# Performance work log

Hardware: AMD Instinct MI355X
Metric: run time of the kernel (lower is better)

## Reference

```python
import jax, jax.numpy as jnp
import numpy as np
import math

B, N, D, H = 4, 2048, 1024, 16
d = D // H
F = 2048                      # field_size
PAD = 8192                    # _next_fast_size(4*F) = 2^13
FB = PAD // 2 + 1             # rfft freq bins
NC = 32                       # spectral-gate control points
EPS = 1e-6                    # feature-map positivity floor


def setup_inputs():
    key = jax.random.key(0)
    ks = jax.random.split(key, 16)
    rn = lambda k, sh, s=0.02: (jax.random.normal(k, sh) * s).astype(jnp.float32)
    eye = jnp.eye(d, dtype=jnp.float32)
    n = jnp.arange(H, dtype=jnp.float32)
    return {
        "x": jax.random.normal(ks[0], (B, N, D), dtype=jnp.float32),
        "w_qkvg": rn(ks[1], (4 * D, D)),
        "b_qkvg": jnp.concatenate([jnp.zeros(3 * D), jnp.full((D,), 2.0)]).astype(jnp.float32),
        "w_out": rn(ks[2], (D, D)),
        "b_out": jnp.zeros((D,), jnp.float32),
        "qfm_w": jnp.stack([eye + rn(ks[3], (d, d)), eye + rn(ks[4], (d, d))]),
        "qfm_b": jnp.zeros((2, d), jnp.float32),
        "kfm_w": jnp.stack([eye + rn(ks[5], (d, d)), eye + rn(ks[6], (d, d))]),
        "kfm_b": jnp.zeros((2, d), jnp.float32),
        "wg_w": rn(ks[7], (1, d)),
        "wg_b": jnp.zeros((1,), jnp.float32),
        "ln_g": jnp.ones((d,), jnp.float32),
        "ln_b": jnp.zeros((d,), jnp.float32),
        "sg_w1": rn(ks[8], (D, D)),
        "sg_b1": jnp.zeros((D,), jnp.float32),
        "sg_w2": rn(ks[9], (H * NC, D), 0.001),
        "sg_b2": jnp.zeros((H * NC,), jnp.float32),
        "wave_freq": (math.pi * (2 * n + 1) / 2).astype(jnp.float32),
        "wave_damp": jnp.full((H,), -0.69, jnp.float32),
        "wave_phase": jnp.linspace(0.0, math.pi, H).astype(jnp.float32),
        "coupling": (jnp.eye(H, dtype=jnp.float32) + rn(ks[10], (H, H), 0.01)),
    }


def _featmap(x, w, b):
    # Hedgehog-style learned positive feature map: depth x (Linear -> ReLU), + eps
    for i in range(w.shape[0]):
        x = jax.nn.relu(x @ w[i].T + b[i])
    return x + EPS


def reference(x, w_qkvg, b_qkvg, w_out, b_out, qfm_w, qfm_b, kfm_w, kfm_b,
              wg_w, wg_b, ln_g, ln_b, sg_w1, sg_b1, sg_w2, sg_b2,
              wave_freq, wave_damp, wave_phase, coupling):
    # fused qkvg projection -> per-head tensors (B,H,N,d)
    qkvg = x @ w_qkvg.T + b_qkvg
    q, k, v, g = [t.reshape(B, N, H, d).transpose(0, 2, 1, 3)
                  for t in jnp.split(qkvg, 4, axis=-1)]
    phi_q = _featmap(q, qfm_w, qfm_b)
    phi_k = _featmap(k, kfm_w, kfm_b)
    wg = jax.nn.sigmoid(k @ wg_w.T + wg_b)  # (B,H,N,1) write gate

    # token -> field position mapping (cached buffers in the original)
    stride = (F - 1) / max(N - 1, 1)
    pos = jnp.clip(jnp.arange(N, dtype=jnp.float32) * stride, 0, F - 2)
    lo = jnp.clip(pos.astype(jnp.int32), 0, F - 2)
    hi = lo + 1
    frac = jnp.clip(pos - lo.astype(jnp.float32), 0.0, 1.0)

    # scatter numerator (gated phi_k*v) + denominator (gated phi_k) streams
    write = jnp.concatenate([wg * phi_k * v, wg * phi_k], axis=-1)  # (B,H,N,2d)
    field = jnp.zeros((B, H, F, 2 * d), jnp.float32)
    field = field.at[:, :, lo, :].add(write * (1.0 - frac)[:, None])
    field = field.at[:, :, hi, :].add(write * frac[:, None])

    # left-aligned causal damped-wave kernel per head
    t = jnp.arange(F, dtype=jnp.float32) / F
    kern = jnp.exp(-jnp.exp(wave_damp)[:, None] * t) * \
           jnp.cos(wave_freq[:, None] * t + wave_phase[:, None])  # (H,F)
    base_fft = jnp.fft.rfft(kern, n=PAD, axis=-1)                 # (H,FB) complex

    # content-adaptive spectral gate from token 0 (causally safe)
    q0 = q[:, :, 0, :]
    mu = q0.mean(-1, keepdims=True)
    var = q0.var(-1, keepdims=True)
    q0 = (q0 - mu) / jnp.sqrt(var + 1e-5) * ln_g + ln_b
    h1 = jax.nn.gelu(q0.reshape(B, H * d) @ sg_w1.T + sg_b1)
    ctrl = (h1 @ sg_w2.T + sg_b2).reshape(B, H, NC)
    ip = jnp.arange(FB, dtype=jnp.float32) * (NC - 1) / (FB - 1)  # align_corners=True
    il = jnp.clip(ip.astype(jnp.int32), 0, NC - 2)
    iw = ip - il.astype(jnp.float32)
    gate = ctrl[:, :, il] * (1.0 - iw) + ctrl[:, :, il + 1] * iw  # (B,H,FB)
    mod = base_fft[None] * (1.0 + gate)                           # (B,H,FB) complex

    # FFT-domain global convolution + head coupling
    conv = jnp.fft.irfft(jnp.fft.rfft(field, n=PAD, axis=2) * mod[..., None],
                         n=PAD, axis=2)[:, :, :F, :]
    conv = jnp.einsum('hg,bgfc->bhfc', coupling, conv)

    # linear-interp read-back at token positions
    y = conv[:, :, lo, :] * (1.0 - frac)[:, None] + conv[:, :, hi, :] * frac[:, None]
    y_num, y_den = y[..., :d], y[..., d:]
    den = jnp.abs(jnp.sum(phi_q * y_den, axis=-1, keepdims=True)) + 1e-4
    out_h = (phi_q * y_num / den) * jax.nn.sigmoid(g)
    return out_h.transpose(0, 2, 1, 3).reshape(B, N, D) @ w_out.T + b_out
```

## Files before the change

### kernel.cpp

```cpp
#include <hip/hip_runtime.h>
#include <math.h>

#define B_   4
#define N_   2048
#define D_   1024
#define H_   16
#define d_   64
#define F_   2048
#define PAD_ 8192
#define FB_  4097
#define NC_  32
#define EPS_ 1e-6f
#define PI_F 3.14159265358979323846f
#define PI_D 3.14159265358979323846

typedef unsigned short ushort_t;
typedef short bf16x8 __attribute__((ext_vector_type(8)));
typedef float f32x4  __attribute__((ext_vector_type(4)));

#define GLD16(gp, lp) __builtin_amdgcn_global_load_lds( \
    (const __attribute__((address_space(1))) unsigned int*)(const void*)(gp), \
    (__attribute__((address_space(3))) unsigned int*)(void*)(lp), 16, 0, 0)

__device__ __forceinline__ ushort_t bf16_rne(float v) {
    unsigned b = __float_as_uint(v);
    unsigned rb = b + 0x7fffu + ((b >> 16) & 1u);
    return (ushort_t)(rb >> 16);
}
__device__ __forceinline__ void split_bf16(float v, ushort_t& h, ushort_t& l) {
    h = bf16_rne(v);
    float fh = __uint_as_float((unsigned)h << 16);
    l = bf16_rne(v - fh);
}

__device__ __forceinline__ float2 cmul(float2 a, float2 w) {
    return make_float2(a.x * w.x - a.y * w.y, a.x * w.y + a.y * w.x);
}
__device__ __forceinline__ float2 cmulc(float2 a, float2 w) {
    return make_float2(a.x * w.x + a.y * w.y, a.y * w.x - a.x * w.y);
}

__global__ __launch_bounds__(256) void kern_twid(float2* __restrict__ twid,
                                                 float2* __restrict__ tw4) {
    int idx = blockIdx.x * 256 + threadIdx.x;
    if (idx < 13 * 4096) {
        const int lh = idx >> 12, t = idx & 4095;
        const int hh = 1 << lh;
        const int j = t & (hh - 1);
        double s, c;
        sincos(-PI_D * (double)j / (double)hh, &s, &c);
        twid[idx] = make_float2((float)c, (float)s);
    } else {
        idx -= 13 * 4096;
        if (idx < 6 * 3072) {
            const int s = idx / 3072;
            const int r = idx - s * 3072;
            const int j = r / 3;
            const int m = r - 3 * j + 1;
            const int q = 1024 >> (2 * s);
            double sn, cs;
            sincos(-2.0 * PI_D * (double)(m * (j & (q - 1))) / (double)(4 * q), &sn, &cs);
            tw4[idx] = make_float2((float)cs, (float)sn);
        }
    }
}

__global__ __launch_bounds__(256) void kern_split3(
        const float* __restrict__ s0, ushort_t* __restrict__ h0, ushort_t* __restrict__ l0, int n0,
        const float* __restrict__ s1, ushort_t* __restrict__ h1, ushort_t* __restrict__ l1, int n1,
        const float* __restrict__ s2, ushort_t* __restrict__ h2, ushort_t* __restrict__ l2, int n2) {
    int i = blockIdx.x * 256 + threadIdx.x;
    const float* s; ushort_t* hh; ushort_t* ll; int k;
    if (i < n0)                { s = s0; hh = h0; ll = l0; k = i; }
    else if (i < n0 + n1)      { s = s1; hh = h1; ll = l1; k = i - n0; }
    else if (i < n0 + n1 + n2) { s = s2; hh = h2; ll = l2; k = i - n0 - n1; }
    else return;
    ushort_t h, l;
    split_bf16(s[k], h, l);
    hh[k] = h; ll[k] = l;
}

__global__ __launch_bounds__(256) void gemm_mfma(
        const ushort_t* __restrict__ Ah, const ushort_t* __restrict__ Al, int lda,
        const ushort_t* __restrict__ Bh, const ushort_t* __restrict__ Bl, int ldb,
        const float* __restrict__ bias, float* __restrict__ C,
        int Nn, int K) {
    __shared__ __align__(16) ushort_t At0[128 * 32];
    __shared__ __align__(16) ushort_t At1[128 * 32];
    __shared__ __align__(16) ushort_t Bt0[128 * 32];
    __shared__ __align__(16) ushort_t Bt1[128 * 32];

    const int tid = threadIdx.x;
    const int wv = tid >> 6, lane = tid & 63;
    const int quad = lane >> 4, lrow = lane & 15;
    const int m0 = blockIdx.y * 128, n0 = blockIdx.x * 128;
    const int mw = (wv >> 1) * 64, nw = (wv & 1) * 64;

    const int srow = lane >> 2;
    const int schunk = (((lane & 3) ^ ((lane >> 3) & 3)) * 8);
    const int qsw = ((quad ^ ((lrow >> 1) & 3)) * 8);

    f32x4 acc[4][4] = {};

    for (int k0 = 0; k0 < K; k0 += 32) {
        {
            const size_t ga = (size_t)(m0 + wv * 32 + srow) * lda + k0 + schunk;
            const size_t gb = (size_t)(n0 + wv * 32 + srow) * ldb + k0 + schunk;
            const size_t ga2 = ga + (size_t)16 * lda;
            const size_t gb2 = gb + (size_t)16 * ldb;
            GLD16(Ah + ga,  &At0[(wv * 32) * 32]);
            GLD16(Ah + ga2, &At0[(wv * 32 + 16) * 32]);
            GLD16(Al + ga,  &At1[(wv * 32) * 32]);
            GLD16(Al + ga2, &At1[(wv * 32 + 16) * 32]);
            GLD16(Bh + gb,  &Bt0[(wv * 32) * 32]);
            GLD16(Bh + gb2, &Bt0[(wv * 32 + 16) * 32]);
            GLD16(Bl + gb,  &Bt1[(wv * 32) * 32]);
            GLD16(Bl + gb2, &Bt1[(wv * 32 + 16) * 32]);
        }
        __syncthreads();

        bf16x8 a0[4], a1[4], b0[4], b1[4];
#pragma unroll
        for (int i = 0; i < 4; ++i) {
            a0[i] = *(const bf16x8*)&At0[(mw + i * 16 + lrow) * 32 + qsw];
            a1[i] = *(const bf16x8*)&At1[(mw + i * 16 + lrow) * 32 + qsw];
            b0[i] = *(const bf16x8*)&Bt0[(nw + i * 16 + lrow) * 32 + qsw];
            b1[i] = *(const bf16x8*)&Bt1[(nw + i * 16 + lrow) * 32 + qsw];
        }
#pragma unroll
        for (int mi = 0; mi < 4; ++mi)
#pragma unroll
            for (int nj = 0; nj < 4; ++nj) {
                acc[mi][nj] = __builtin_amdgcn_mfma_f32_16x16x32_bf16(a0[mi], b0[nj], acc[mi][nj], 0, 0, 0);
                acc[mi][nj] = __builtin_amdgcn_mfma_f32_16x16x32_bf16(a0[mi], b1[nj], acc[mi][nj], 0, 0, 0);
                acc[mi][nj] = __builtin_amdgcn_mfma_f32_16x16x32_bf16(a1[mi], b0[nj], acc[mi][nj], 0, 0, 0);
            }
        __syncthreads();
    }

#pragma unroll
    for (int mi = 0; mi < 4; ++mi) {
        const int row = m0 + mw + mi * 16 + quad * 4;
#pragma unroll
        for (int nj = 0; nj < 4; ++nj) {
            const int col = n0 + nw + nj * 16 + lrow;
            const float bv = bias[col];
#pragma unroll
            for (int r = 0; r < 4; ++r)
                C[(size_t)(row + r) * Nn + col] = acc[mi][nj][r] + bv;
        }
    }
}

__device__ __forceinline__ float gelu_f(float x) {
    return 0.5f * x * (1.f + tanhf(0.7978845608028654f * (x + 0.044715f * x * x * x)));
}

__global__ __launch_bounds__(256) void kern_gemv4(const float* __restrict__ A,
                                                  const float* __restrict__ W,
                                                  const float* __restrict__ bias,
                                                  float* __restrict__ C,
                                                  int Nn, int act) {
    const int tid = threadIdx.x;
    const int wv = tid >> 6, lane = tid & 63;
    const int col = blockIdx.x * 4 + wv;
    const float* wp = W + (size_t)col * D_;
    float a0 = 0.f, a1 = 0.f, a2 = 0.f, a3 = 0.f;
#pragma unroll
    for (int i = 0; i < 16; ++i) {
        int k = lane + i * 64;
        float w = wp[k];
        a0 += A[k] * w;
        a1 += A[D_ + k] * w;
        a2 += A[2 * D_ + k] * w;
        a3 += A[3 * D_ + k] * w;
    }
    for (int m = 1; m < 64; m <<= 1) {
        a0 += __shfl_xor(a0, m);
        a1 += __shfl_xor(a1, m);
        a2 += __shfl_xor(a2, m);
        a3 += __shfl_xor(a3, m);
    }
    if (lane == 0) {
        float bv = bias[col];
        float v0 = a0 + bv, v1 = a1 + bv, v2 = a2 + bv, v3 = a3 + bv;
        if (act) { v0 = gelu_f(v0); v1 = gelu_f(v1); v2 = gelu_f(v2); v3 = gelu_f(v3); }
        C[0 * Nn + col] = v0;
        C[1 * Nn + col] = v1;
        C[2 * Nn + col] = v2;
        C[3 * Nn + col] = v3;
    }
}

__global__ __launch_bounds__(256) void kern_feat(float* __restrict__ qkvg,
                                                 const float* __restrict__ qfm_w,
                                                 const float* __restrict__ qfm_b,
                                                 const float* __restrict__ kfm_w,
                                                 const float* __restrict__ kfm_b,
                                                 const float* __restrict__ wg_w,
                                                 const float* __restrict__ wg_b,
                                                 float* __restrict__ field) {
    __shared__ __align__(16) float in_t[64][68];
    __shared__ __align__(16) float tmp[64][68];
    __shared__ __align__(16) float wbuf[64][68];
    __shared__ __align__(16) float bsm[64];
    __shared__ float wsm[64];
    __shared__ float wgbuf[64];

    const int tid = threadIdx.x;
    const int lane = tid & 63, grp = tid >> 6;
    const int n0 = blockIdx.x * 64;
    const int h = blockIdx.y, b = blockIdx.z;
    const size_t rowbase = (size_t)(b * N_ + n0) * 4096;

    const int lr4 = tid >> 4;
    const int lc4 = (tid & 15) * 4;

    const int rg = lane >> 4;
    const int cg4 = (lane & 15) * 4;
    const int rbase = grp * 16 + rg * 4;

#define LOAD64x64(dst, off) \
    for (int it = 0; it < 4; ++it) { \
        int r = lr4 + it * 16; \
        float4 v = *(const float4*)&qkvg[rowbase + (size_t)r * 4096 + (off) + lc4]; \
        *(float4*)&dst[r][lc4] = v; \
    }

#define MLP2_ACC(srcarr) \
    f32x4 acc[4] = {}; \
    for (int c4 = 0; c4 < 64; c4 += 4) { \
        f32x4 wv0 = *(const f32x4*)&wbuf[c4 + 0][cg4]; \
        f32x4 wv1 = *(const f32x4*)&wbuf[c4 + 1][cg4]; \
        f32x4 wv2 = *(const f32x4*)&wbuf[c4 + 2][cg4]; \
        f32x4 wv3 = *(const f32x4*)&wbuf[c4 + 3][cg4]; \
        _Pragma("unroll") for (int rr = 0; rr < 4; ++rr) { \
            f32x4 iv = *(const f32x4*)&srcarr[rbase + rr][c4]; \
            acc[rr] += wv0 * iv[0]; \
            acc[rr] += wv1 * iv[1]; \
            acc[rr] += wv2 * iv[2]; \
            acc[rr] += wv3 * iv[3]; \
        } \
    }

#define MLP2_STORE_LDS(dstarr, EPSV) { \
    f32x4 b4 = *(const f32x4*)&bsm[cg4]; \
    _Pragma("unroll") for (int rr = 0; rr < 4; ++rr) { \
        f32x4 v = acc[rr] + b4; \
        _Pragma("unroll") for (int k = 0; k < 4; ++k) v[k] = fmaxf(v[k], 0.f) + (EPSV); \
        *(f32x4*)&dstarr[rbase + rr][cg4] = v; } }

    LOAD64x64(in_t, D_ + h * 64)
    for (int it = 0; it < 16; ++it) {
        int r = grp + 4 * it;
        wbuf[lane][r] = kfm_w[(size_t)r * 64 + lane];
    }
    if (tid < 64) { bsm[tid] = kfm_b[tid]; wsm[tid] = wg_w[tid]; }
    __syncthreads();
    if (tid < 64) {
        float s = 0.f;
        for (int c4 = 0; c4 < 64; c4 += 4) {
            float4 iv = *(const float4*)&in_t[tid][c4];
            s += iv.x * wsm[c4] + iv.y * wsm[c4 + 1] + iv.z * wsm[c4 + 2] + iv.w * wsm[c4 + 3];
        }
        s += wg_b[0];
        wgbuf[tid] = 1.f / (1.f + expf(-s));
    }
    {
        MLP2_ACC(in_t)
        MLP2_STORE_LDS(tmp, 0.f)
    }
    __syncthreads();
    for (int it = 0; it < 16; ++it) {
        int r = grp + 4 * it;
        wbuf[lane][r] = kfm_w[(size_t)(64 + r) * 64 + lane];
    }
    if (tid < 64) bsm[tid] = kfm_b[64 + tid];
    __syncthreads();
    {
        MLP2_ACC(tmp)
        MLP2_STORE_LDS(in_t, EPS_)
    }
    __syncthreads();
    LOAD64x64(tmp, 2 * D_ + h * 64)
    __syncthreads();

    {
        float* frow = field + (size_t)(b * H_ + h) * 128 * F_;
        const bool last = (n0 == N_ - 64);
        for (int c = grp; c < 128; c += 4) {
            int i = lane;
            float v = (c < 64) ? wgbuf[i] * in_t[i][c] * tmp[i][c]
                               : wgbuf[i] * in_t[i][c - 64];
            if (last) {
                if (i == 62) {
                    float v2 = (c < 64) ? wgbuf[63] * in_t[63][c] * tmp[63][c]
                                        : wgbuf[63] * in_t[63][c - 64];
                    v += v2;
                } else if (i == 63) v = 0.f;
            }
            frow[(size_t)c * F_ + n0 + i] = v;
        }
    }
    __syncthreads();

    LOAD64x64(in_t, h * 64)
    for (int it = 0; it < 16; ++it) {
        int r = grp + 4 * it;
        wbuf[lane][r] = qfm_w[(size_t)r * 64 + lane];
    }
    if (tid < 64) bsm[tid] = qfm_b[tid];
    __syncthreads();
    {
        MLP2_ACC(in_t)
        MLP2_STORE_LDS(tmp, 0.f)
    }
    __syncthreads();
    for (int it = 0; it < 16; ++it) {
        int r = grp + 4 * it;
        wbuf[lane][r] = qfm_w[(size_t)(64 + r) * 64 + lane];
    }
    if (tid < 64) bsm[tid] = qfm_b[64 + tid];
    __syncthreads();
    {
        MLP2_ACC(tmp)
        f32x4 b4 = *(const f32x4*)&bsm[cg4];
#pragma unroll
        for (int rr = 0; rr < 4; ++rr) {
            f32x4 v = acc[rr] + b4;
#pragma unroll
            for (int k = 0; k < 4; ++k) v[k] = fmaxf(v[k], 0.f) + EPS_;
            *(f32x4*)&qkvg[rowbase + (size_t)(rbase + rr) * 4096 + D_ + h * 64 + cg4] = v;
        }
    }
#undef LOAD64x64
#undef MLP2_ACC
#undef MLP2_STORE_LDS
}

__global__ void kern_ln(const float* __restrict__ qkvg,
                        const float* __restrict__ ln_g,
                        const float* __restrict__ ln_b,
                        float* __restrict__ q0n) {
    const int bh = blockIdx.x, c = threadIdx.x;
    const int b = bh >> 4, h = bh & 15;
    float x = qkvg[(size_t)(b * N_) * 4096 + h * 64 + c];
    float mu = x;
    for (int m = 1; m < 64; m <<= 1) mu += __shfl_xor(mu, m);
    mu *= (1.f / 64.f);
    float dv = (x - mu) * (x - mu);
    for (int m = 1; m < 64; m <<= 1) dv += __shfl_xor(dv, m);
    float var = dv * (1.f / 64.f);
    q0n[b * 1024 + h * 64 + c] = (x - mu) * rsqrtf(var + 1e-5f) * ln_g[c] + ln_b[c];
}

template <int NT>
__device__ __forceinline__ void fft_fwd_dif_t(float* xr, float* xi, int tid, int logn,
                                              const float2* __restrict__ twid) {
    const int nb = 1 << (logn - 1);
    for (int lh = logn - 1; lh >= 0; --lh) {
        const int hh = 1 << lh;
        const float2* tws = twid + lh * 4096;
        for (int t = tid; t < nb; t += NT) {
            int j = t & (hh - 1);
            int i1 = ((t >> lh) << (lh + 1)) | j;
            int i2 = i1 + hh;
            float2 tw = tws[t];
            float ar = xr[i1], ai = xi[i1];
            float br = xr[i2], bi = xi[i2];
            xr[i1] = ar + br; xi[i1] = ai + bi;
            float tr = ar - br, ti = ai - bi;
            xr[i2] = tr * tw.x - ti * tw.y;
            xi[i2] = tr * tw.y + ti * tw.x;
        }
        __syncthreads();
    }
}

template <int NT>
__device__ __forceinline__ void fft_inv_dit_t(float* xr, float* xi, int tid, int logn,
                                              const float2* __restrict__ twid) {
    const int nb = 1 << (logn - 1);
    for (int lh = 0; lh < logn; ++lh) {
        const int hh = 1 << lh;
        const float2* tws = twid + lh * 4096;
        for (int t = tid; t < nb; t += NT) {
            int j = t & (hh - 1);
            int i1 = ((t >> lh) << (lh + 1)) | j;
            int i2 = i1 + hh;
            float2 tw = tws[t];
            float br = xr[i2], bi = xi[i2];
            float tr = br * tw.x + bi * tw.y;
            float ti = bi * tw.x - br * tw.y;
            float ar = xr[i1], ai = xi[i1];
            xr[i1] = ar + tr; xi[i1] = ai + ti;
            xr[i2] = ar - tr; xi[i2] = ai - ti;
        }
        __syncthreads();
    }
}

#define ZIDX(i) ((i) + ((i) >> 4))

template <int NT>
__device__ __forceinline__ void fft4_fwd(float2* z, int tid,
                                         const float2* __restrict__ tw4) {
#pragma unroll
    for (int s = 0; s < 6; ++s) {
        const int q = 1024 >> (2 * s);
        const int qq = q + (q >> 4);
        const float2* tws = tw4 + s * 3072;
        for (int t = tid; t < 1024; t += NT) {
            int j = t & (q - 1);
            int base = ((t & ~(q - 1)) << 2) | j;
            int i0, i1, i2, i3;
            if (q >= 16) { i0 = ZIDX(base); i1 = i0 + qq; i2 = i1 + qq; i3 = i2 + qq; }
            else { i0 = ZIDX(base); i1 = ZIDX(base + q); i2 = ZIDX(base + 2 * q); i3 = ZIDX(base + 3 * q); }
            float2 a = z[i0], b = z[i1], c = z[i2], d = z[i3];
            float2 s0 = make_float2(a.x + c.x, a.y + c.y);
            float2 s1 = make_float2(a.x - c.x, a.y - c.y);
            float2 s2 = make_float2(b.x + d.x, b.y + d.y);
            float2 s3 = make_float2(b.x - d.x, b.y - d.y);
            float2 m1 = make_float2(s1.x + s3.y, s1.y - s3.x);
            float2 m2 = make_float2(s0.x - s2.x, s0.y - s2.y);
            float2 m3 = make_float2(s1.x - s3.y, s1.y + s3.x);
            z[i0] = make_float2(s0.x + s2.x, s0.y + s2.y);
            z[i1] = cmul(m1, tws[3 * j + 0]);
            z[i2] = cmul(m2, tws[3 * j + 1]);
            z[i3] = cmul(m3, tws[3 * j + 2]);
        }
        __syncthreads();
    }
}

template <int NT>
__device__ __forceinline__ void fft4_inv(float2* z, int tid,
                                         const float2* __restrict__ tw4) {
#pragma unroll
    for (int s = 5; s >= 0; --s) {
        const int q = 1024 >> (2 * s);
        const int qq = q + (q >> 4);
        const float2* tws = tw4 + s * 3072;
        for (int t = tid; t < 1024; t += NT) {
            int j = t & (q - 1);
            int base = ((t & ~(q - 1)) << 2) | j;
            int i0, i1, i2, i3;
            if (q >= 16) { i0 = ZIDX(base); i1 = i0 + qq; i2 = i1 + qq; i3 = i2 + qq; }
            else { i0 = ZIDX(base); i1 = ZIDX(base + q); i2 = ZIDX(base + 2 * q); i3 = ZIDX(base + 3 * q); }
            float2 a = z[i0];
            float2 b = cmulc(z[i1], tws[3 * j + 0]);
            float2 c = cmulc(z[i2], tws[3 * j + 1]);
            float2 d = cmulc(z[i3], tws[3 * j + 2]);
            float2 p0 = make_float2(a.x + c.x, a.y + c.y);
            float2 p1 = make_float2(a.x - c.x, a.y - c.y);
            float2 p2 = make_float2(b.x + d.x, b.y + d.y);
            float2 p3 = make_float2(b.x - d.x, b.y - d.y);
            z[i0] = make_float2(p0.x + p2.x, p0.y + p2.y);
            z[i1] = make_float2(p1.x - p3.y, p1.y + p3.x);
            z[i2] = make_float2(p0.x - p2.x, p0.y - p2.y);
            z[i3] = make_float2(p1.x + p3.y, p1.y - p3.x);
        }
        __syncthreads();
    }
}

__global__ __launch_bounds__(1024) void kern_prep(const float* __restrict__ freq,
                                                  const float* __restrict__ damp,
                                                  const float* __restrict__ phase,
                                                  const float* __restrict__ ctrl,
                                                  const float2* __restrict__ twid,
                                                  const float2* __restrict__ tw4,
                                                  float* __restrict__ GBR) {
    __shared__ float sm[2 * PAD_];
    float* xr = sm;
    float* xi = sm + PAD_;
    const int bh = blockIdx.x, tid = threadIdx.x;
    const int b = bh >> 4, h = bh & 15;

    const float fr = freq[h], ed = expf(damp[h]), ph = phase[h];
    for (int f = tid; f < PAD_; f += 1024) {
        float v = 0.f;
        if (f < F_) {
            float t = (float)f / (float)F_;
            v = expf(-ed * t) * cosf(fr * t + ph);
        }
        xr[f] = v; xi[f] = 0.f;
    }
    __syncthreads();
    fft_fwd_dif_t<1024>(xr, xi, tid, 13, twid);

    const float* cp = ctrl + b * (H_ * NC_) + h * NC_;
    for (int j = tid; j < PAD_; j += 1024) {
        int k = (int)(__brev((unsigned)j) >> 19);
        int kk = min(k, PAD_ - k);
        float ip = (float)kk * ((float)(NC_ - 1) / (float)(FB_ - 1));
        int il = min((int)ip, NC_ - 2);
        float iw = ip - (float)il;
        float m = 1.f + cp[il] * (1.f - iw) + cp[il + 1] * iw;
        xr[j] *= m;
        xi[j] *= m;
    }
    __syncthreads();
    fft_inv_dit_t<1024>(xr, xi, tid, 13, twid);

    float g[4];
    const float sc = 1.f / (float)PAD_;
#pragma unroll
    for (int u = 0; u < 4; ++u) {
        int j = tid + u * 1024;
        g[u] = ((j < 2048) ? xr[j] : xr[j + 4096]) * sc;
    }
    __syncthreads();
    float2* z = (float2*)sm;
#pragma unroll
    for (int u = 0; u < 4; ++u) {
        int j = tid + u * 1024;
        z[ZIDX(j)] = make_float2(g[u], 0.f);
    }
    __syncthreads();
    fft4_fwd<1024>(z, tid, tw4);
    for (int j = tid; j < 4096; j += 1024) {
        float2 v = z[ZIDX(j)];
        GBR[((size_t)bh * 4096 + j) * 2 + 0] = v.x;
        GBR[((size_t)bh * 4096 + j) * 2 + 1] = v.y;
    }
}

__global__ __launch_bounds__(512) void kern_conv4(float* __restrict__ field,
                                                  const float* __restrict__ GBR,
                                                  const float2* __restrict__ tw4) {
    __shared__ float2 z[4351];
    const int tid = threadIdx.x;
    const int bh = blockIdx.x >> 6, cp = blockIdx.x & 63;
    float* rowx = field + ((size_t)bh * 128 + 2 * cp) * F_;
    float* rowy = rowx + F_;

    for (int f = tid; f < 2048; f += 512) {
        z[ZIDX(f)] = make_float2(rowx[f], rowy[f]);
        z[ZIDX(f + 2048)] = make_float2(0.f, 0.f);
    }
    __syncthreads();

    fft4_fwd<512>(z, tid, tw4);

    {
        const float2* G = (const float2*)(GBR) + (size_t)bh * 4096;
        for (int j = tid; j < 4096; j += 512) {
            int zi = ZIDX(j);
            z[zi] = cmul(z[zi], G[j]);
        }
    }
    __syncthreads();

    fft4_inv<512>(z, tid, tw4);

    const float s = 1.f / 4096.f;
    for (int f = tid; f < 2048; f += 512) {
        float2 v = z[ZIDX(f)];
        rowx[f] = v.x * s;
        rowy[f] = v.y * s;
    }
}

__global__ __launch_bounds__(1024) void kern_combine(float* __restrict__ qkvg,
                                                     const float* __restrict__ field,
                                                     const float* __restrict__ coupling) {
    __shared__ float cpl[16][16];
    __shared__ float sbuf[2][128][17];
    const int tid = threadIdx.x;
    if (tid < 256) cpl[tid >> 4][tid & 15] = coupling[tid];
    const int lane = tid & 63, wv = tid >> 6;
    const int n = blockIdx.x * 16 + wv;
    const int b = blockIdx.y;
    const int f0 = blockIdx.x * 16;
    const int fi = min(n, F_ - 2) - f0;
    const size_t row = (size_t)(b * N_ + n) * 4096;

    const int lc = tid >> 3, lk = (tid & 7) * 2;
    const float* fb = field + (size_t)b * 16 * 128 * F_;

    float2 rv = *(const float2*)&fb[(size_t)lc * F_ + f0 + lk];
    __syncthreads();
    sbuf[0][lc][lk] = rv.x; sbuf[0][lc][lk + 1] = rv.y;

    float ynum[16], yden[16];
#pragma unroll
    for (int hh = 0; hh < 16; ++hh) { ynum[hh] = 0.f; yden[hh] = 0.f; }

    for (int g = 0; g < 16; ++g) {
        if (g < 15)
            rv = *(const float2*)&fb[((size_t)(g + 1) * 128 + lc) * F_ + f0 + lk];
        __syncthreads();
        const float nv = sbuf[g & 1][lane][fi];
        const float dv = sbuf[g & 1][64 + lane][fi];
#pragma unroll
        for (int hh = 0; hh < 16; ++hh) {
            const float cg = cpl[hh][g];
            ynum[hh] += cg * nv;
            yden[hh] += cg * dv;
        }
        if (g < 15) { sbuf[(g + 1) & 1][lc][lk] = rv.x; sbuf[(g + 1) & 1][lc][lk + 1] = rv.y; }
    }

    ushort_t* rp = (ushort_t*)(qkvg + row);
#pragma unroll
    for (int hh = 0; hh < 16; ++hh) {
        float pq = qkvg[row + D_ + hh * 64 + lane];
        float gv = qkvg[row + 3 * D_ + hh * 64 + lane];
        float s = pq * yden[hh];
        for (int m = 1; m < 64; m <<= 1) s += __shfl_xor(s, m);
        float den = fabsf(s) + 1e-4f;
        float o = pq * ynum[hh] / den * (1.f / (1.f + expf(-gv)));
        ushort_t oh, ol;
        split_bf16(o, oh, ol);
        rp[hh * 64 + lane] = oh;
        rp[1024 + hh * 64 + lane] = ol;
    }
}

extern "C" void kernel_launch(void* const* d_in, const int* in_sizes, int n_in,
                              void* d_out, int out_size, void* d_ws, size_t ws_size,
                              hipStream_t stream) {
    const float* x      = (const float*)d_in[0];
    const float* w_qkvg = (const float*)d_in[1];
    const float* b_qkvg = (const float*)d_in[2];
    const float* w_out  = (const float*)d_in[3];
    const float* b_out  = (const float*)d_in[4];
    const float* qfm_w  = (const float*)d_in[5];
    const float* qfm_b  = (const float*)d_in[6];
    const float* kfm_w  = (const float*)d_in[7];
    const float* kfm_b  = (const float*)d_in[8];
    const float* wg_w   = (const float*)d_in[9];
    const float* wg_b   = (const float*)d_in[10];
    const float* ln_g   = (const float*)d_in[11];
    const float* ln_b   = (const float*)d_in[12];
    const float* sg_w1  = (const float*)d_in[13];
    const float* sg_b1  = (const float*)d_in[14];
    const float* sg_w2  = (const float*)d_in[15];
    const float* sg_b2  = (const float*)d_in[16];
    const float* wfreq  = (const float*)d_in[17];
    const float* wdamp  = (const float*)d_in[18];
    const float* wphase = (const float*)d_in[19];
    const float* coup   = (const float*)d_in[20];

    float* ws = (float*)d_ws;
    float*  qkvg   = ws;
    float*  field  = ws + 33554432;
    float*  GBR    = ws + 50593792;
    float2* twid   = (float2*)(ws + 51118080);
    float*  q0n    = ws + 51224576;
    float*  h1     = ws + 51228672;
    float*  ctrl   = ws + 51232768;
    ushort_t* wouth = (ushort_t*)(ws + 51234816);
    ushort_t* woutl = (ushort_t*)(ws + 51759104);
    float2* tw4    = (float2*)(ws + 52283392);

    ushort_t* xh  = (ushort_t*)(field);
    ushort_t* xl  = (ushort_t*)(field + 4194304);
    ushort_t* wqh = (ushort_t*)(field + 8388608);
    ushort_t* wql = (ushort_t*)(field + 10485760);

    kern_twid<<<(13 * 4096 + 6 * 3072) / 256, 256, 0, stream>>>(twid, tw4);
    kern_split3<<<(B_ * N_ * D_ + 4 * D_ * D_ + D_ * D_) / 256, 256, 0, stream>>>(
        x, xh, xl, B_ * N_ * D_,
        w_qkvg, wqh, wql, 4 * D_ * D_,
        w_out, wouth, woutl, D_ * D_);

    gemm_mfma<<<dim3(4096 / 128, 8192 / 128), 256, 0, stream>>>(
        xh, xl, D_, wqh, wql, D_, b_qkvg, qkvg, 4 * D_, D_);

    kern_ln<<<B_ * H_, 64, 0, stream>>>(qkvg, ln_g, ln_b, q0n);
    kern_gemv4<<<D_ / 4, 256, 0, stream>>>(q0n, sg_w1, sg_b1, h1, D_, 1);
    kern_gemv4<<<(H_ * NC_) / 4, 256, 0, stream>>>(h1, sg_w2, sg_b2, ctrl, H_ * NC_, 0);

    kern_prep<<<B_ * H_, 1024, 0, stream>>>(wfreq, wdamp, wphase, ctrl, twid, tw4, GBR);

    kern_feat<<<dim3(N_ / 64, H_, B_), 256, 0, stream>>>(
        qkvg, qfm_w, qfm_b, kfm_w, kfm_b, wg_w, wg_b, field);

    kern_conv4<<<B_ * H_ * 64, 512, 0, stream>>>(field, GBR, tw4);

    kern_combine<<<dim3(N_ / 16, B_), 1024, 0, stream>>>(qkvg, field, coup);

    gemm_mfma<<<dim3(1024 / 128, 8192 / 128), 256, 0, stream>>>(
        (ushort_t*)qkvg, (ushort_t*)qkvg + 1024, 8192,
        wouth, woutl, D_, b_out, (float*)d_out, D_, D_);
}
```

Measured before the change: 699.1 us.

## Prune zero-padded FFT stage, fuse final radix-4 stage with spectral multiply

The convolution kernel no longer zero-fills the upper half of the padded signal. Its first radix-4 stage is specialised so it reads only the nonzero half, and the last forward stage is fused with the pointwise multiply by the precomputed kernel spectrum, saving shared-memory passes and a barrier. The 1/4096 normalisation moves into the prep kernel's stored spectrum. The QKVG GEMM is also split into four launches over row chunks, which adds launch overhead and may change cache behaviour.

New measurement: 705.9 us. Within noise of the previous version (+1.0%).

```diff
diff --git a/kernel.cpp b/kernel.cpp
--- a/kernel.cpp
+++ b/kernel.cpp
@@ -402,11 +402,11 @@
 
 #define ZIDX(i) ((i) + ((i) >> 4))
 
-template <int NT>
-__device__ __forceinline__ void fft4_fwd(float2* z, int tid,
-                                         const float2* __restrict__ tw4) {
-#pragma unroll
-    for (int s = 0; s < 6; ++s) {
+template <int NT, int SBEG, int SEND>
+__device__ __forceinline__ void fft4_fwd_stages(float2* z, int tid,
+                                                const float2* __restrict__ tw4) {
+#pragma unroll
+    for (int s = SBEG; s < SEND; ++s) {
         const int q = 1024 >> (2 * s);
         const int qq = q + (q >> 4);
         const float2* tws = tw4 + s * 3072;
@@ -518,11 +518,26 @@
         z[ZIDX(j)] = make_float2(g[u], 0.f);
     }
     __syncthreads();
-    fft4_fwd<1024>(z, tid, tw4);
-    for (int j = tid; j < 4096; j += 1024) {
-        float2 v = z[ZIDX(j)];
-        GBR[((size_t)bh * 4096 + j) * 2 + 0] = v.x;
-        GBR[((size_t)bh * 4096 + j) * 2 + 1] = v.y;
+    fft4_fwd_stages<1024, 0, 5>(z, tid, tw4);
+    {
+        const float sc2 = 1.f / 4096.f;
+        const int t = tid;
+        const int base = t << 2;
+        float2 a = z[ZIDX(base)], bq = z[ZIDX(base + 1)];
+        float2 c = z[ZIDX(base + 2)], dq = z[ZIDX(base + 3)];
+        float2 s0 = make_float2(a.x + c.x, a.y + c.y);
+        float2 s1 = make_float2(a.x - c.x, a.y - c.y);
+        float2 s2 = make_float2(bq.x + dq.x, bq.y + dq.y);
+        float2 s3 = make_float2(bq.x - dq.x, bq.y - dq.y);
+        float2 o0 = make_float2(s0.x + s2.x, s0.y + s2.y);
+        float2 o1 = make_float2(s1.x + s3.y, s1.y - s3.x);
+        float2 o2 = make_float2(s0.x - s2.x, s0.y - s2.y);
+        float2 o3 = make_float2(s1.x - s3.y, s1.y + s3.x);
+        float2* Gp = (float2*)GBR + (size_t)bh * 4096 + base;
+        Gp[0] = make_float2(o0.x * sc2, o0.y * sc2);
+        Gp[1] = make_float2(o1.x * sc2, o1.y * sc2);
+        Gp[2] = make_float2(o2.x * sc2, o2.y * sc2);
+        Gp[3] = make_float2(o3.x * sc2, o3.y * sc2);
     }
 }
 
@@ -535,30 +550,56 @@
     float* rowx = field + ((size_t)bh * 128 + 2 * cp) * F_;
     float* rowy = rowx + F_;
 
-    for (int f = tid; f < 2048; f += 512) {
+    for (int f = tid; f < 2048; f += 512)
         z[ZIDX(f)] = make_float2(rowx[f], rowy[f]);
-        z[ZIDX(f + 2048)] = make_float2(0.f, 0.f);
-    }
-    __syncthreads();
-
-    fft4_fwd<512>(z, tid, tw4);
+    __syncthreads();
+
+    {
+        const float2* tws = tw4;
+        for (int t = tid; t < 1024; t += 512) {
+            int i0 = ZIDX(t), i1 = i0 + 1088, i2 = i1 + 1088, i3 = i2 + 1088;
+            float2 a = z[i0], b = z[i1];
+            float2 m1 = make_float2(a.x + b.y, a.y - b.x);
+            float2 m2 = make_float2(a.x - b.x, a.y - b.y);
+            float2 m3 = make_float2(a.x - b.y, a.y + b.x);
+            z[i0] = make_float2(a.x + b.x, a.y + b.y);
+            z[i1] = cmul(m1, tws[3 * t + 0]);
+            z[i2] = cmul(m2, tws[3 * t + 1]);
+            z[i3] = cmul(m3, tws[3 * t + 2]);
+        }
+        __syncthreads();
+    }
+
+    fft4_fwd_stages<512, 1, 5>(z, tid, tw4);
 
     {
         const float2* G = (const float2*)(GBR) + (size_t)bh * 4096;
-        for (int j = tid; j < 4096; j += 512) {
-            int zi = ZIDX(j);
-            z[zi] = cmul(z[zi], G[j]);
-        }
-    }
-    __syncthreads();
+        for (int t = tid; t < 1024; t += 512) {
+            int base = t << 2;
+            int i0 = ZIDX(base), i1 = ZIDX(base + 1), i2 = ZIDX(base + 2), i3 = ZIDX(base + 3);
+            float2 a = z[i0], b = z[i1], c = z[i2], d = z[i3];
+            float2 s0 = make_float2(a.x + c.x, a.y + c.y);
+            float2 s1 = make_float2(a.x - c.x, a.y - c.y);
+            float2 s2 = make_float2(b.x + d.x, b.y + d.y);
+            float2 s3 = make_float2(b.x - d.x, b.y - d.y);
+            float2 o0 = make_float2(s0.x + s2.x, s0.y + s2.y);
+            float2 o1 = make_float2(s1.x + s3.y, s1.y - s3.x);
+            float2 o2 = make_float2(s0.x - s2.x, s0.y - s2.y);
+            float2 o3 = make_float2(s1.x - s3.y, s1.y + s3.x);
+            z[i0] = cmul(o0, G[base + 0]);
+            z[i1] = cmul(o1, G[base + 1]);
+            z[i2] = cmul(o2, G[base + 2]);
+            z[i3] = cmul(o3, G[base + 3]);
+        }
+        __syncthreads();
+    }
 
     fft4_inv<512>(z, tid, tw4);
 
-    const float s = 1.f / 4096.f;
     for (int f = tid; f < 2048; f += 512) {
         float2 v = z[ZIDX(f)];
-        rowx[f] = v.x * s;
-        rowy[f] = v.y * s;
+        rowx[f] = v.x;
+        rowy[f] = v.y;
     }
 }
 
@@ -666,8 +707,12 @@
         w_qkvg, wqh, wql, 4 * D_ * D_,
         w_out, wouth, woutl, D_ * D_);
 
-    gemm_mfma<<<dim3(4096 / 128, 8192 / 128), 256, 0, stream>>>(
-        xh, xl, D_, wqh, wql, D_, b_qkvg, qkvg, 4 * D_, D_);
+    for (int l = 0; l < 4; ++l) {
+        const size_t aoff = (size_t)l * 2048 * D_;
+        gemm_mfma<<<dim3(4096 / 128, 2048 / 128), 256, 0, stream>>>(
+            xh + aoff, xl + aoff, D_, wqh, wql, D_, b_qkvg,
+            qkvg + (size_t)l * 2048 * 4096, 4 * D_, D_);
+    }
 
     kern_ln<<<B_ * H_, 64, 0, stream>>>(qkvg, ln_g, ln_b, q0n);
     kern_gemv4<<<D_ / 4, 256, 0, stream>>>(q0n, sg_w1, sg_b1, h1, D_, 1);
```
